# Optimization experiments

Measured on AMD Instinct MI355X. Metric: run time of the kernel, lower is better.

The kernel has to match this reference:

```python
import jax, jax.numpy as jnp
import numpy as np

N_NODES = 4096
N_EDGES = 500000
N_PAIRS = 2000000
EDGE_DIM = 16
MAX_PATH = 5


def setup_inputs() -> dict:
    key = jax.random.key(0)
    k1, k2, k3, k4, k5 = jax.random.split(key, 5)
    x = jax.random.normal(k1, (N_NODES, EDGE_DIM), dtype=jnp.float32)
    edge_attr = jax.random.normal(k2, (N_EDGES, EDGE_DIM), dtype=jnp.float32)
    path_idx = jax.random.randint(k3, (N_PAIRS, MAX_PATH), 0, N_EDGES, dtype=jnp.int64)
    path_lens = jax.random.randint(k4, (N_PAIRS,), 0, MAX_PATH + 1, dtype=jnp.int64)
    pair_id = jnp.arange(N_PAIRS, dtype=jnp.int64)
    # learned parameter: edge_weights [max_path_distance, edge_dim]
    edge_weights = jax.random.normal(k5, (MAX_PATH, EDGE_DIM), dtype=jnp.float32)
    return {"x": x, "edge_attr": edge_attr, "edge_weights": edge_weights,
            "path_idx": path_idx, "path_lens": path_lens, "pair_id": pair_id}


def reference(x, edge_attr, edge_weights, path_idx, path_lens, pair_id):
    N = x.shape[0]
    L = edge_weights.shape[0]  # max_path_distance
    # valid-position mask for each ragged path, padded to length L
    mask = (jnp.arange(L)[None, :] < path_lens[:, None]).astype(edge_attr.dtype)  # [P, L]
    gathered = edge_attr[path_idx]  # [P, L, D] ragged gather of edge features
    # per-hop dot with learned per-hop weight vector, i.e. (w_l * e_l).sum(dim=1)
    dots = jnp.einsum('pld,ld->pl', gathered, edge_weights)  # [P, L]
    s = jnp.sum(dots * mask, axis=1)  # [P]
    cnt = path_lens.astype(edge_attr.dtype)
    # mean over valid hops; empty path -> NaN in torch -> nan_to_num -> 0
    mean = jnp.where(cnt > 0, s / jnp.maximum(cnt, 1.0), jnp.zeros_like(s))
    src = pair_id % N
    dst = pair_id // N  # unique (src, dst) pairs by construction
    cij = jnp.zeros((N, N), dtype=edge_attr.dtype).at[src, dst].set(mean)
    return cij
```

## Files before the change

kernel.cpp:

```cpp
#include <hip/hip_runtime.h>
#include <hip/hip_fp16.h>

#define NNODES 4096
#define NEDGES 500000
#define NPAIRS 2000000
#define EDIM   16
#define LMAX   5

__global__ __launch_bounds__(256) void dots_kernel(
    const float* __restrict__ edge_attr,
    const float* __restrict__ ew,
    __half* __restrict__ dots) {
  __shared__ float w[LMAX * EDIM];
  int tid = threadIdx.x;
  if (tid < LMAX * EDIM) w[tid] = ew[tid];
  __syncthreads();

  int e0 = (blockIdx.x * 256 + tid) * 2;
  if (e0 >= NEDGES) return;

  const float4* ra = (const float4*)(edge_attr + (size_t)e0 * EDIM);
  float4 a0 = ra[0], a1 = ra[1], a2 = ra[2], a3 = ra[3];
  float4 b0 = ra[4], b1 = ra[5], b2 = ra[6], b3 = ra[7];
  float va[16] = {a0.x, a0.y, a0.z, a0.w, a1.x, a1.y, a1.z, a1.w,
                  a2.x, a2.y, a2.z, a2.w, a3.x, a3.y, a3.z, a3.w};
  float vb[16] = {b0.x, b0.y, b0.z, b0.w, b1.x, b1.y, b1.z, b1.w,
                  b2.x, b2.y, b2.z, b2.w, b3.x, b3.y, b3.z, b3.w};
#pragma unroll
  for (int l = 0; l < LMAX; ++l) {
    float da = 0.f, db = 0.f;
#pragma unroll
    for (int k = 0; k < EDIM; ++k) {
      da += va[k] * w[l * EDIM + k];
      db += vb[k] * w[l * EDIM + k];
    }
    __half2 h;
    h.x = __float2half(da);
    h.y = __float2half(db);
    *(__half2*)(dots + (size_t)l * NEDGES + e0) = h;
  }
}

__global__ __launch_bounds__(256) void mean_kernel(
    const int* __restrict__ path_idx,
    const int* __restrict__ path_lens,
    const __half* __restrict__ dots,
    float* __restrict__ mean) {
  int p = blockIdx.x * 256 + threadIdx.x;
  if (p >= NPAIRS) return;

  int len = __builtin_nontemporal_load(path_lens + p);
  len = min(max(len, 0), LMAX);

  const int* row = path_idx + (size_t)p * LMAX;
  int i0 = __builtin_nontemporal_load(row + 0);
  int i1 = __builtin_nontemporal_load(row + 1);
  int i2 = __builtin_nontemporal_load(row + 2);
  int i3 = __builtin_nontemporal_load(row + 3);
  int i4 = __builtin_nontemporal_load(row + 4);

  float s = 0.f;
  if (len > 0) s += __half2float(dots[i0]);
  if (len > 1) s += __half2float(dots[1 * NEDGES + i1]);
  if (len > 2) s += __half2float(dots[2 * NEDGES + i2]);
  if (len > 3) s += __half2float(dots[3 * NEDGES + i3]);
  if (len > 4) s += __half2float(dots[4 * NEDGES + i4]);

  mean[p] = (len > 0) ? (s / (float)len) : 0.f;
}

__global__ __launch_bounds__(256) void expand_transpose(
    const float* __restrict__ mean,
    float* __restrict__ out) {
  const int dst0 = blockIdx.x * 64;
  const int src0 = blockIdx.y * 64;
  const int tid = threadIdx.x;

  if (dst0 * NNODES >= NPAIRS) {
    float4 z = {0.f, 0.f, 0.f, 0.f};
#pragma unroll
    for (int i = 0; i < 4; ++i) {
      int slot = tid + i * 256;
      int a = slot >> 4;
      int c = slot & 15;
      ((float4*)(out + (size_t)(src0 + a) * NNODES + dst0))[c] = z;
    }
    return;
  }

  __shared__ float tile[64][65];

#pragma unroll
  for (int i = 0; i < 4; ++i) {
    int slot = tid + i * 256;
    int a = slot >> 4;
    int c = slot & 15;
    int p = (dst0 + a) * NNODES + src0 + 4 * c;
    float4 v;
    if (p < NPAIRS) v = *(const float4*)(mean + p);
    else { v.x = 0.f; v.y = 0.f; v.z = 0.f; v.w = 0.f; }
    tile[a][4 * c + 0] = v.x;
    tile[a][4 * c + 1] = v.y;
    tile[a][4 * c + 2] = v.z;
    tile[a][4 * c + 3] = v.w;
  }
  __syncthreads();
#pragma unroll
  for (int i = 0; i < 4; ++i) {
    int slot = tid + i * 256;
    int a = slot >> 4;
    int c = slot & 15;
    float4 v;
    v.x = tile[4 * c + 0][a];
    v.y = tile[4 * c + 1][a];
    v.z = tile[4 * c + 2][a];
    v.w = tile[4 * c + 3][a];
    ((float4*)(out + (size_t)(src0 + a) * NNODES + dst0))[c] = v;
  }
}

__global__ __launch_bounds__(256) void scatter_kernel(
    const float* __restrict__ edge_attr,
    const float* __restrict__ ew,
    const int* __restrict__ path_idx,
    const int* __restrict__ path_lens,
    float* __restrict__ out) {
  __shared__ float w[LMAX * EDIM];
  if (threadIdx.x < LMAX * EDIM) w[threadIdx.x] = ew[threadIdx.x];
  __syncthreads();

  int p = blockIdx.x * 256 + threadIdx.x;
  if (p >= NPAIRS) return;

  int len = path_lens[p];
  len = min(max(len, 0), LMAX);

  const int* row = path_idx + (size_t)p * LMAX;
  float s = 0.f;
  for (int l = 0; l < len; ++l) {
    int idx = row[l];
    const float4* r = (const float4*)(edge_attr + (size_t)idx * EDIM);
    float4 a0 = r[0], a1 = r[1], a2 = r[2], a3 = r[3];
    const float* wl = &w[l * EDIM];
    s += a0.x * wl[0] + a0.y * wl[1] + a0.z * wl[2] + a0.w * wl[3] +
         a1.x * wl[4] + a1.y * wl[5] + a1.z * wl[6] + a1.w * wl[7] +
         a2.x * wl[8] + a2.y * wl[9] + a2.z * wl[10] + a2.w * wl[11] +
         a3.x * wl[12] + a3.y * wl[13] + a3.z * wl[14] + a3.w * wl[15];
  }
  float m = (len > 0) ? (s / (float)len) : 0.f;
  int src = p & (NNODES - 1);
  int dst = p >> 12;
  out[(size_t)src * NNODES + dst] = m;
}

extern "C" void kernel_launch(void* const* d_in, const int* in_sizes, int n_in,
                              void* d_out, int out_size, void* d_ws, size_t ws_size,
                              hipStream_t stream) {
  const float* edge_attr = (const float*)d_in[1];
  const float* edge_w    = (const float*)d_in[2];
  const int*   path_idx  = (const int*)d_in[3];
  const int*   path_lens = (const int*)d_in[4];
  float* out = (float*)d_out;

  const size_t need = (size_t)NPAIRS * sizeof(float) +
                      (size_t)LMAX * NEDGES * sizeof(__half);

  if (ws_size >= need) {
    float* mean = (float*)d_ws;
    __half* dots = (__half*)((char*)d_ws + (size_t)NPAIRS * sizeof(float));

    dots_kernel<<<(NEDGES / 2 + 255) / 256, 256, 0, stream>>>(edge_attr, edge_w, dots);
    mean_kernel<<<(NPAIRS + 255) / 256, 256, 0, stream>>>(path_idx, path_lens, dots, mean);
    dim3 grid(64, 64), block(256, 1);
    expand_transpose<<<grid, block, 0, stream>>>(mean, out);
  } else {
    hipMemsetAsync(d_out, 0, (size_t)out_size * sizeof(float), stream);
    scatter_kernel<<<(NPAIRS + 255) / 256, 256, 0, stream>>>(
        edge_attr, edge_w, path_idx, path_lens, out);
  }
}
```

Baseline: 175.6 us.

## Fuse mean computation into transpose kernel and drop mean buffer

Removes the separate mean kernel and its intermediate buffer. The transpose kernel now computes each pair's mean on the fly, reading path indices and lengths as vectorized 128-bit nontemporal loads covering four pairs. The aim is to save one launch and a write plus re-read of the mean array. The swapped grid axes change the order in which tiles are scheduled, and per-thread work grows in the transpose.

Measured after the change: 179.4 us. 1.02x slower.

```diff
diff --git a/kernel.cpp b/kernel.cpp
--- a/kernel.cpp
+++ b/kernel.cpp
@@ -6,6 +6,12 @@
 #define NPAIRS 2000000
 #define EDIM   16
 #define LMAX   5
+
+typedef int v4i __attribute__((ext_vector_type(4)));
+
+__device__ __forceinline__ v4i ntload4(const int* p) {
+  return __builtin_nontemporal_load((const v4i*)p);
+}
 
 __global__ __launch_bounds__(256) void dots_kernel(
     const float* __restrict__ edge_attr,
@@ -41,39 +47,26 @@
   }
 }
 
-__global__ __launch_bounds__(256) void mean_kernel(
+__device__ __forceinline__ float pair_mean(
+    const __half* __restrict__ dots, int len,
+    int i0, int i1, int i2, int i3, int i4) {
+  len = min(max(len, 0), LMAX);
+  float v0 = (len > 0) ? __half2float(dots[i0]) : 0.f;
+  float v1 = (len > 1) ? __half2float(dots[1 * NEDGES + i1]) : 0.f;
+  float v2 = (len > 2) ? __half2float(dots[2 * NEDGES + i2]) : 0.f;
+  float v3 = (len > 3) ? __half2float(dots[3 * NEDGES + i3]) : 0.f;
+  float v4 = (len > 4) ? __half2float(dots[4 * NEDGES + i4]) : 0.f;
+  float s = ((v0 + v1) + (v2 + v3)) + v4;
+  return (len > 0) ? s / (float)len : 0.f;
+}
+
+__global__ __launch_bounds__(256) void fused_mean_transpose(
     const int* __restrict__ path_idx,
     const int* __restrict__ path_lens,
     const __half* __restrict__ dots,
-    float* __restrict__ mean) {
-  int p = blockIdx.x * 256 + threadIdx.x;
-  if (p >= NPAIRS) return;
-
-  int len = __builtin_nontemporal_load(path_lens + p);
-  len = min(max(len, 0), LMAX);
-
-  const int* row = path_idx + (size_t)p * LMAX;
-  int i0 = __builtin_nontemporal_load(row + 0);
-  int i1 = __builtin_nontemporal_load(row + 1);
-  int i2 = __builtin_nontemporal_load(row + 2);
-  int i3 = __builtin_nontemporal_load(row + 3);
-  int i4 = __builtin_nontemporal_load(row + 4);
-
-  float s = 0.f;
-  if (len > 0) s += __half2float(dots[i0]);
-  if (len > 1) s += __half2float(dots[1 * NEDGES + i1]);
-  if (len > 2) s += __half2float(dots[2 * NEDGES + i2]);
-  if (len > 3) s += __half2float(dots[3 * NEDGES + i3]);
-  if (len > 4) s += __half2float(dots[4 * NEDGES + i4]);
-
-  mean[p] = (len > 0) ? (s / (float)len) : 0.f;
-}
-
-__global__ __launch_bounds__(256) void expand_transpose(
-    const float* __restrict__ mean,
     float* __restrict__ out) {
-  const int dst0 = blockIdx.x * 64;
-  const int src0 = blockIdx.y * 64;
+  const int src0 = blockIdx.x * 64;
+  const int dst0 = blockIdx.y * 64;
   const int tid = threadIdx.x;
 
   if (dst0 * NNODES >= NPAIRS) {
@@ -96,9 +89,20 @@
     int a = slot >> 4;
     int c = slot & 15;
     int p = (dst0 + a) * NNODES + src0 + 4 * c;
-    float4 v;
-    if (p < NPAIRS) v = *(const float4*)(mean + p);
-    else { v.x = 0.f; v.y = 0.f; v.z = 0.f; v.w = 0.f; }
+    float4 v = {0.f, 0.f, 0.f, 0.f};
+    if (p < NPAIRS) {
+      v4i ln = ntload4(path_lens + p);
+      const int* q = path_idx + (size_t)p * LMAX;
+      v4i A = ntload4(q);
+      v4i B = ntload4(q + 4);
+      v4i C = ntload4(q + 8);
+      v4i D = ntload4(q + 12);
+      v4i E = ntload4(q + 16);
+      v.x = pair_mean(dots, ln[0], A[0], A[1], A[2], A[3], B[0]);
+      v.y = pair_mean(dots, ln[1], B[1], B[2], B[3], C[0], C[1]);
+      v.z = pair_mean(dots, ln[2], C[2], C[3], D[0], D[1], D[2]);
+      v.w = pair_mean(dots, ln[3], D[3], E[0], E[1], E[2], E[3]);
+    }
     tile[a][4 * c + 0] = v.x;
     tile[a][4 * c + 1] = v.y;
     tile[a][4 * c + 2] = v.z;
@@ -162,17 +166,14 @@
   const int*   path_lens = (const int*)d_in[4];
   float* out = (float*)d_out;
 
-  const size_t need = (size_t)NPAIRS * sizeof(float) +
-                      (size_t)LMAX * NEDGES * sizeof(__half);
+  const size_t need = (size_t)LMAX * NEDGES * sizeof(__half);
 
   if (ws_size >= need) {
-    float* mean = (float*)d_ws;
-    __half* dots = (__half*)((char*)d_ws + (size_t)NPAIRS * sizeof(float));
+    __half* dots = (__half*)d_ws;
 
     dots_kernel<<<(NEDGES / 2 + 255) / 256, 256, 0, stream>>>(edge_attr, edge_w, dots);
-    mean_kernel<<<(NPAIRS + 255) / 256, 256, 0, stream>>>(path_idx, path_lens, dots, mean);
     dim3 grid(64, 64), block(256, 1);
-    expand_transpose<<<grid, block, 0, stream>>>(mean, out);
+    fused_mean_transpose<<<grid, block, 0, stream>>>(path_idx, path_lens, dots, out);
   } else {
     hipMemsetAsync(d_out, 0, (size_t)out_size * sizeof(float), stream);
     scatter_kernel<<<(NPAIRS + 255) / 256, 256, 0, stream>>>(
```
